# Performance work log

Measured on AMD Instinct MI355X. Metric: run time of the kernel, lower is better.

Reference implementation:

```python
import jax, jax.numpy as jnp
import numpy as np
import math

B, L, OBS, ACT = 2, 1024, 64, 16
OE, AE, RE, TE = 512, 256, 128, 128
C, H, NL, FF = 1024, 16, 4, 4096
DH = C // H


def setup_inputs():
    key = jax.random.key(0)
    ks = jax.random.split(key, 20)
    def nrm(k, shape, std=1.0):
        return jax.random.normal(k, shape, jnp.float32) * std
    kb = jax.random.split(ks[19], 12)
    return {
        'obs_seq': nrm(ks[0], (B, L, OBS)),
        'act_seq': nrm(ks[1], (B, L, ACT)),
        'rew_seq': nrm(ks[2], (B, L, 1)),
        'obs_W': nrm(ks[3], (OBS, OE), OBS ** -0.5), 'obs_b': jnp.zeros((OE,)),
        'act_W': nrm(ks[4], (ACT, AE), ACT ** -0.5), 'act_b': jnp.zeros((AE,)),
        'rew_W': nrm(ks[5], (1, RE), 1.0), 'rew_b': jnp.zeros((RE,)),
        'tr_W': nrm(ks[6], (OBS, TE), OBS ** -0.5), 'tr_b': jnp.zeros((TE,)),
        'bn_gamma': jnp.ones((OBS,)), 'bn_beta': jnp.zeros((OBS,)),
        'ln1_w': jnp.ones((NL, C)), 'ln1_b': jnp.zeros((NL, C)),
        'qkv_W': nrm(kb[0], (NL, C, 3 * C), C ** -0.5), 'qkv_b': jnp.zeros((NL, 3 * C)),
        'out_W': nrm(kb[1], (NL, C, C), C ** -0.5), 'out_b': jnp.zeros((NL, C)),
        'ln2_w': jnp.ones((NL, C)), 'ln2_b': jnp.zeros((NL, C)),
        'fc_W': nrm(kb[2], (NL, C, FF), C ** -0.5), 'fc_b': jnp.zeros((NL, FF)),
        'pj_W': nrm(kb[3], (NL, FF, C), FF ** -0.5), 'pj_b': jnp.zeros((NL, C)),
    }


def _ln(x, w, b):
    m = x.mean(-1, keepdims=True)
    v = ((x - m) ** 2).mean(-1, keepdims=True)
    return (x - m) * jax.lax.rsqrt(v + 1e-5) * w + b


def _forward(obs_seq, act_seq, rew_seq, obs_W, obs_b, act_W, act_b, rew_W, rew_b,
             tr_W, tr_b, bn_gamma, bn_beta, ln1_w, ln1_b, qkv_W, qkv_b, out_W, out_b,
             ln2_w, ln2_b, fc_W, fc_b, pj_W, pj_b):
    # transition branch: prepend first obs, take deltas; BatchNorm1d in training
    # mode uses biased batch stats over (batch, time) per channel.
    full_obs = jnp.concatenate([obs_seq[:, :1], obs_seq], axis=1)  # (B, L+1, OBS)
    obs2 = full_obs[:, :-1]
    tran = full_obs[:, 1:] - full_obs[:, :-1]  # (B, L, OBS)
    tm = tran.mean((0, 1))
    tv = ((tran - tm) ** 2).mean((0, 1))
    tran = (tran - tm) * jax.lax.rsqrt(tv + 1e-5) * bn_gamma + bn_beta
    # encoder_activation is identity
    enc = jnp.concatenate([
        obs2 @ obs_W + obs_b,
        act_seq @ act_W + act_b,
        rew_seq @ rew_W + rew_b,
        tran @ tr_W + tr_b,
    ], axis=-1)  # (B, L, C)
    mask = jnp.tril(jnp.ones((L, L), dtype=bool))

    def block(x, p):
        l1w, l1b, qW, qb, oW, ob, l2w, l2b, fW, fb, pW, pb = p
        h = _ln(x, l1w, l1b)
        q, k, v = jnp.split(h @ qW + qb, 3, axis=-1)
        q, k, v = (t.reshape(B, L, H, DH).transpose(0, 2, 1, 3) for t in (q, k, v))
        s = jnp.einsum('bhqd,bhkd->bhqk', q, k) / math.sqrt(DH)
        s = jnp.where(mask, s, -jnp.inf)
        a = jax.nn.softmax(s, axis=-1)
        o = jnp.einsum('bhqk,bhkd->bhqd', a, v).transpose(0, 2, 1, 3).reshape(B, L, C)
        x = x + o @ oW + ob  # residual + out_proj
        h2 = _ln(x, l2w, l2b)
        x = x + jax.nn.relu(h2 @ fW + fb) @ pW + pb  # MLP residual
        return x, None

    x, _ = jax.lax.scan(block, enc, (ln1_w, ln1_b, qkv_W, qkv_b, out_W, out_b,
                                     ln2_w, ln2_b, fc_W, fc_b, pj_W, pj_b))
    return jnp.tanh(x)


def reference(obs_seq, act_seq, rew_seq, obs_W, obs_b, act_W, act_b, rew_W, rew_b,
              tr_W, tr_b, bn_gamma, bn_beta, ln1_w, ln1_b, qkv_W, qkv_b, out_W, out_b,
              ln2_w, ln2_b, fc_W, fc_b, pj_W, pj_b):
    return _forward(obs_seq, act_seq, rew_seq, obs_W, obs_b, act_W, act_b, rew_W, rew_b,
                    tr_W, tr_b, bn_gamma, bn_beta, ln1_w, ln1_b, qkv_W, qkv_b, out_W, out_b,
                    ln2_w, ln2_b, fc_W, fc_b, pj_W, pj_b)
```

## Files before the change

kernel.cpp:

```cpp
#include <hip/hip_runtime.h>
#include <hip/hip_bf16.h>
#include <math.h>

constexpr int kB   = 2;
constexpr int kL   = 1024;
constexpr int kOBS = 64;
constexpr int kACT = 16;
constexpr int kC   = 1024;
constexpr int kH   = 16;
constexpr int kDH  = 64;
constexpr int kFF  = 4096;
constexpr int kNL  = 4;
constexpr int kRows = kB * kL;
constexpr int kOE = 512, kAE = 256, kRE = 128, kTE = 128;

typedef _Float16 f16x8 __attribute__((ext_vector_type(8)));
typedef _Float16 f16x4 __attribute__((ext_vector_type(4)));
typedef float    f32x4 __attribute__((ext_vector_type(4)));

__device__ __forceinline__ unsigned short f2h(float x) {
    return __builtin_bit_cast(unsigned short, (_Float16)x);
}
__device__ __forceinline__ void gload_lds16(const void* g, void* l) {
    __builtin_amdgcn_global_load_lds(
        (const __attribute__((address_space(1))) unsigned int*)g,
        (__attribute__((address_space(3))) unsigned int*)l, 16, 0, 0);
}

__global__ __launch_bounds__(256) void tran_stats_kernel(
    const float* __restrict__ obs, float* __restrict__ tm, float* __restrict__ tv)
{
    const int f = blockIdx.x;
    const int tid = threadIdx.x;
    float sum = 0.f, sq = 0.f;
    for (int r = tid; r < kRows; r += 256) {
        const int t = r & (kL - 1);
        float d = 0.f;
        if (t > 0) {
            const float cur  = obs[(size_t)r * kOBS + f];
            const float prev = obs[(size_t)(r - 1) * kOBS + f];
            d = cur - prev;
        }
        sum += d; sq += d * d;
    }
    for (int off = 32; off > 0; off >>= 1) {
        sum += __shfl_down(sum, off);
        sq  += __shfl_down(sq, off);
    }
    __shared__ float sa[4], sb[4];
    if ((tid & 63) == 0) { sa[tid >> 6] = sum; sb[tid >> 6] = sq; }
    __syncthreads();
    if (tid == 0) {
        const float ts = sa[0] + sa[1] + sa[2] + sa[3];
        const float tq = sb[0] + sb[1] + sb[2] + sb[3];
        const float m = ts / (float)kRows;
        tm[f] = m;
        tv[f] = tq / (float)kRows - m * m;
    }
}

__global__ __launch_bounds__(256) void encode_kernel(
    const float* __restrict__ obs, const float* __restrict__ act, const float* __restrict__ rew,
    const float* __restrict__ obs_W, const float* __restrict__ obs_b,
    const float* __restrict__ act_W, const float* __restrict__ act_b,
    const float* __restrict__ rew_W, const float* __restrict__ rew_b,
    const float* __restrict__ tr_W,  const float* __restrict__ tr_b,
    const float* __restrict__ bn_g,  const float* __restrict__ bn_b,
    const float* __restrict__ tm,    const float* __restrict__ tv,
    float* __restrict__ enc)
{
    const int row = blockIdx.x;
    const int t = row & (kL - 1);
    const int tid = threadIdx.x;
    __shared__ float s_obs2[kOBS];
    __shared__ float s_tran[kOBS];
    __shared__ float s_act[kACT];
    __shared__ float s_rew;
    if (tid < kOBS) {
        const float cur  = obs[(size_t)row * kOBS + tid];
        const float prev = (t > 0) ? obs[(size_t)(row - 1) * kOBS + tid] : cur;
        s_obs2[tid] = prev;
        const float tr = cur - prev;
        s_tran[tid] = (tr - tm[tid]) * rsqrtf(tv[tid] + 1e-5f) * bn_g[tid] + bn_b[tid];
    } else if (tid < kOBS + kACT) {
        s_act[tid - kOBS] = act[(size_t)row * kACT + (tid - kOBS)];
    } else if (tid == kOBS + kACT) {
        s_rew = rew[row];
    }
    __syncthreads();
    float* er = enc + (size_t)row * kC;
    #pragma unroll
    for (int s = 0; s < 4; ++s) {
        const int c = tid + s * 256;
        float v;
        if (c < kOE) {
            v = obs_b[c];
            #pragma unroll
            for (int k = 0; k < kOBS; ++k) v += s_obs2[k] * obs_W[k * kOE + c];
        } else if (c < kOE + kAE) {
            const int cc = c - kOE;
            v = act_b[cc];
            #pragma unroll
            for (int k = 0; k < kACT; ++k) v += s_act[k] * act_W[k * kAE + cc];
        } else if (c < kOE + kAE + kRE) {
            const int cc = c - (kOE + kAE);
            v = s_rew * rew_W[cc] + rew_b[cc];
        } else {
            const int cc = c - (kOE + kAE + kRE);
            v = tr_b[cc];
            #pragma unroll
            for (int k = 0; k < kOBS; ++k) v += s_tran[k] * tr_W[k * kTE + cc];
        }
        er[c] = v;
    }
}

__global__ __launch_bounds__(256) void ln_kernel(
    const float* __restrict__ x, const float* __restrict__ w,
    const float* __restrict__ b, unsigned short* __restrict__ out)
{
    const int row = blockIdx.x;
    const int tid = threadIdx.x;
    const float4 xv = *reinterpret_cast<const float4*>(&x[(size_t)row * kC + tid * 4]);
    float s = xv.x + xv.y + xv.z + xv.w;
    float q = xv.x * xv.x + xv.y * xv.y + xv.z * xv.z + xv.w * xv.w;
    for (int off = 32; off > 0; off >>= 1) {
        s += __shfl_down(s, off);
        q += __shfl_down(q, off);
    }
    __shared__ float sa[4], sb[4];
    if ((tid & 63) == 0) { sa[tid >> 6] = s; sb[tid >> 6] = q; }
    __syncthreads();
    const float ts = sa[0] + sa[1] + sa[2] + sa[3];
    const float tq = sb[0] + sb[1] + sb[2] + sb[3];
    const float mean = ts * (1.f / kC);
    const float var  = tq * (1.f / kC) - mean * mean;
    const float rstd = rsqrtf(var + 1e-5f);
    const float4 wv = *reinterpret_cast<const float4*>(&w[tid * 4]);
    const float4 bv = *reinterpret_cast<const float4*>(&b[tid * 4]);
    ushort4 o;
    o.x = f2h((xv.x - mean) * rstd * wv.x + bv.x);
    o.y = f2h((xv.y - mean) * rstd * wv.y + bv.y);
    o.z = f2h((xv.z - mean) * rstd * wv.z + bv.z);
    o.w = f2h((xv.w - mean) * rstd * wv.w + bv.w);
    *reinterpret_cast<ushort4*>(&out[(size_t)row * kC + tid * 4]) = o;
}

__device__ __forceinline__ void convT_tile(
    const float* __restrict__ W, unsigned short* __restrict__ WT,
    int K, int N, int k0, int n0, int tid)
{
    __shared__ unsigned short t[64][68];
    const int r = tid >> 4, c4 = (tid & 15) * 4;
    #pragma unroll
    for (int s = 0; s < 4; ++s) {
        const int rr = r + s * 16;
        const float4 v = *reinterpret_cast<const float4*>(&W[(size_t)(k0 + rr) * N + n0 + c4]);
        t[rr][c4 + 0] = f2h(v.x);
        t[rr][c4 + 1] = f2h(v.y);
        t[rr][c4 + 2] = f2h(v.z);
        t[rr][c4 + 3] = f2h(v.w);
    }
    __syncthreads();
    #pragma unroll
    for (int s = 0; s < 4; ++s) {
        const int rn = r + s * 16;
        ushort4 o;
        o.x = t[c4 + 0][rn];
        o.y = t[c4 + 1][rn];
        o.z = t[c4 + 2][rn];
        o.w = t[c4 + 3][rn];
        *reinterpret_cast<ushort4*>(&WT[(size_t)(n0 + rn) * K + k0 + c4]) = o;
    }
}

__global__ __launch_bounds__(256) void convert_layer_kernel(
    const float* __restrict__ qW, const float* __restrict__ oW,
    const float* __restrict__ fW, const float* __restrict__ pW,
    unsigned short* __restrict__ qWT, unsigned short* __restrict__ oWT,
    unsigned short* __restrict__ fWT, unsigned short* __restrict__ pWT)
{
    int bid = blockIdx.x;
    const int tid = threadIdx.x;
    if (bid < 768)  {
        convT_tile(qW, qWT, 1024, 3072, (bid / 48) * 64, (bid % 48) * 64, tid);
    } else if (bid < 1024) {
        bid -= 768;
        convT_tile(oW, oWT, 1024, 1024, (bid / 16) * 64, (bid % 16) * 64, tid);
    } else if (bid < 2048) {
        bid -= 1024;
        convT_tile(fW, fWT, 1024, 4096, (bid / 64) * 64, (bid % 64) * 64, tid);
    } else {
        bid -= 2048;
        convT_tile(pW, pWT, 4096, 1024, (bid / 16) * 64, (bid % 16) * 64, tid);
    }
}

template<int RELU, int RES, int MODE>
__global__ __launch_bounds__(256) void gemm_f16_kernel(
    const unsigned short* __restrict__ A,
    const unsigned short* __restrict__ BT,
    const float* __restrict__ bias,
    float* __restrict__ Cf, unsigned short* __restrict__ Ch,
    unsigned short* __restrict__ Cv,
    int M, int N, int K)
{
    __shared__ __align__(16) unsigned short As[2][128 * 64];
    __shared__ __align__(16) unsigned short Bs[2][128 * 64];
    const int tid = threadIdx.x;
    const int lane = tid & 63;
    const int wv   = tid >> 6;
    const int wr = wv >> 1, wc = wv & 1;

    const int nx  = gridDim.x;
    const int nxy = gridDim.x * gridDim.y;
    int flat = blockIdx.x + nx * blockIdx.y + nxy * blockIdx.z;
    const int cpx = (nxy * gridDim.z) >> 3;
    flat = (flat & 7) * cpx + (flat >> 3);
    const int bx = flat % nx;
    const int by = (flat / nx) % gridDim.y;
    const int bz = flat / nxy;

    const int bm = by * 128;
    const int bn = bx * 128;
    const int ksz  = K / gridDim.z;
    const int kbeg = bz * ksz;
    const int kend = kbeg + ksz;

    const int grow = tid >> 3;
    const int gs   = (tid & 7) ^ (grow & 7);

    const int fr = lane & 15;
    const int kb = lane >> 4;

    auto stage = [&](int k0, int buf) {
        #pragma unroll
        for (int c = 0; c < 4; ++c) {
            gload_lds16(A  + (size_t)(bm + c * 32 + grow) * K + k0 + gs * 8,
                        (char*)&As[buf][0] + c * 4096 + wv * 1024);
            gload_lds16(BT + (size_t)(bn + c * 32 + grow) * K + k0 + gs * 8,
                        (char*)&Bs[buf][0] + c * 4096 + wv * 1024);
        }
    };

    f32x4 acc[4][4] = {};

    stage(kbeg, 0);
    __syncthreads();
    int cur = 0;
    for (int k0 = kbeg; k0 < kend; k0 += 64) {
        f16x8 a[2][4], b[2][4];
        #pragma unroll
        for (int kf = 0; kf < 2; ++kf) {
            #pragma unroll
            for (int m = 0; m < 4; ++m) {
                const int row = wr * 64 + m * 16 + fr;
                a[kf][m] = *reinterpret_cast<const f16x8*>(
                    &As[cur][row * 64 + (((kf * 4 + kb) ^ (row & 7)) * 8)]);
            }
            #pragma unroll
            for (int n = 0; n < 4; ++n) {
                const int row = wc * 64 + n * 16 + fr;
                b[kf][n] = *reinterpret_cast<const f16x8*>(
                    &Bs[cur][row * 64 + (((kf * 4 + kb) ^ (row & 7)) * 8)]);
            }
        }
        if (k0 + 64 < kend) stage(k0 + 64, cur ^ 1);
        #pragma unroll
        for (int kf = 0; kf < 2; ++kf)
            #pragma unroll
            for (int m = 0; m < 4; ++m)
                #pragma unroll
                for (int n = 0; n < 4; ++n)
                    acc[m][n] = __builtin_amdgcn_mfma_f32_16x16x32_f16(
                        a[kf][m], b[kf][n], acc[m][n], 0, 0, 0);

        __syncthreads();
        cur ^= 1;
    }

    const int fq = lane >> 4;
    if (MODE == 4) {
        const bool addb = (bz == 0);
        #pragma unroll
        for (int n = 0; n < 4; ++n) {
            const int c = bn + wc * 64 + n * 16 + fr;
            const float bv = addb ? bias[c] : 0.f;
            #pragma unroll
            for (int m = 0; m < 4; ++m) {
                #pragma unroll
                for (int j = 0; j < 4; ++j) {
                    const int r = bm + wr * 64 + m * 16 + fq * 4 + j;
                    atomicAdd(&Cf[(size_t)r * N + c], acc[m][n][j] + bv);
                }
            }
        }
        return;
    }
    if (MODE == 2) {
        if (bn < 2 * kC) {
            #pragma unroll
            for (int n = 0; n < 4; ++n) {
                const int c = bn + wc * 64 + n * 16 + fr;
                const float bv = bias[c];
                #pragma unroll
                for (int m = 0; m < 4; ++m) {
                    #pragma unroll
                    for (int j = 0; j < 4; ++j) {
                        const int r = bm + wr * 64 + m * 16 + fq * 4 + j;
                        Ch[(size_t)r * (2 * kC) + c] = f2h(acc[m][n][j] + bv);
                    }
                }
            }
        } else {
            #pragma unroll
            for (int n = 0; n < 4; ++n) {
                const int c  = bn + wc * 64 + n * 16 + fr;
                const int cc = c - 2 * kC;
                const int hh = cc >> 6, dd = cc & 63;
                const float bv = bias[c];
                #pragma unroll
                for (int m = 0; m < 4; ++m) {
                    const int rr = bm + wr * 64 + m * 16 + fq * 4;
                    const int bb = rr >> 10, t0 = rr & 1023;
                    f16x4 pk;
                    #pragma unroll
                    for (int j = 0; j < 4; ++j) pk[j] = (_Float16)(acc[m][n][j] + bv);
                    *reinterpret_cast<f16x4*>(
                        &Cv[((size_t)(bb * kH + hh) * kDH + dd) * kL + t0]) = pk;
                }
            }
        }
        return;
    }
    #pragma unroll
    for (int n = 0; n < 4; ++n) {
        const int c = bn + wc * 64 + n * 16 + fr;
        const float bv = bias[c];
        #pragma unroll
        for (int m = 0; m < 4; ++m) {
            #pragma unroll
            for (int j = 0; j < 4; ++j) {
                const int r = bm + wr * 64 + m * 16 + fq * 4 + j;
                float v = acc[m][n][j] + bv;
                if (RES)  v += Cf[(size_t)r * N + c];
                if (RELU) v = fmaxf(v, 0.f);
                if (MODE == 1) Ch[(size_t)r * N + c] = f2h(v);
                else           Cf[(size_t)r * N + c] = v;
            }
        }
    }
}

__device__ __forceinline__ int swz(int row, int slot) {
    return row * 64 + ((slot ^ (row & 7)) * 8);
}

__global__ __launch_bounds__(256) void attn_mfma_kernel(
    const unsigned short* __restrict__ qk,
    const unsigned short* __restrict__ vt,
    unsigned short* __restrict__ o)
{
    const int bid = blockIdx.x;
    const int bh  = bid & 31;
    const int qb  = ((bid >> 5) + bh) & 15;
    const int b   = bh >> 4;
    const int h   = bh & 15;
    const int tid  = threadIdx.x;
    const int lane = tid & 63;
    const int wv   = tid >> 6;
    const int fr = lane & 15;
    const int g  = lane >> 4;

    __shared__ __align__(16) unsigned short Ks[64 * 64];
    __shared__ __align__(16) unsigned short Vts[64 * 64];
    __shared__ __align__(16) unsigned short Ps[64 * 64];

    const int qlo = qb * 64;
    const int qg_row = qlo + wv * 16 + fr;

    f16x8 qfrag[2];
    {
        const unsigned short* qg = &qk[(size_t)(b * kL + qg_row) * (2 * kC) + h * kDH];
        #pragma unroll
        for (int kf = 0; kf < 2; ++kf) {
            f16x8 v = *reinterpret_cast<const f16x8*>(&qg[(kf * 4 + g) * 8]);
            #pragma unroll
            for (int i = 0; i < 8; ++i) v[i] *= (_Float16)0.125f;
            qfrag[kf] = v;
        }
    }

    const int sr = tid >> 2;
    const int ss = tid & 3;
    const unsigned short* kbase = &qk[(size_t)(b * kL) * (2 * kC) + kC + h * kDH];
    const unsigned short* vbase = &vt[(size_t)(b * kH + h) * kDH * kL];

    f16x8 kc0 = *reinterpret_cast<const f16x8*>(&kbase[(size_t)sr * (2 * kC) + ss * 8]);
    f16x8 kc1 = *reinterpret_cast<const f16x8*>(&kbase[(size_t)sr * (2 * kC) + (ss + 4) * 8]);
    f16x8 vc0 = *reinterpret_cast<const f16x8*>(&vbase[(size_t)sr * kL + ss * 8]);
    f16x8 vc1 = *reinterpret_cast<const f16x8*>(&vbase[(size_t)sr * kL + (ss + 4) * 8]);

    float m = -INFINITY, l = 0.f;
    f32x4 acc_o[4] = {};

    for (int k0 = 0; k0 <= qlo; k0 += 64) {
        asm volatile("s_waitcnt lgkmcnt(0)" ::: "memory");
        __builtin_amdgcn_sched_barrier(0);
        __builtin_amdgcn_s_barrier();
        __builtin_amdgcn_sched_barrier(0);

        *reinterpret_cast<f16x8*>(&Ks[swz(sr, ss)])      = kc0;
        *reinterpret_cast<f16x8*>(&Ks[swz(sr, ss + 4)])  = kc1;
        *reinterpret_cast<f16x8*>(&Vts[swz(sr, ss)])     = vc0;
        *reinterpret_cast<f16x8*>(&Vts[swz(sr, ss + 4)]) = vc1;

        if (k0 + 64 <= qlo) {
            kc0 = *reinterpret_cast<const f16x8*>(&kbase[(size_t)(k0 + 64 + sr) * (2 * kC) + ss * 8]);
            kc1 = *reinterpret_cast<const f16x8*>(&kbase[(size_t)(k0 + 64 + sr) * (2 * kC) + (ss + 4) * 8]);
            vc0 = *reinterpret_cast<const f16x8*>(&vbase[(size_t)sr * kL + k0 + 64 + ss * 8]);
            vc1 = *reinterpret_cast<const f16x8*>(&vbase[(size_t)sr * kL + k0 + 64 + (ss + 4) * 8]);
        }

        asm volatile("s_waitcnt lgkmcnt(0)" ::: "memory");
        __builtin_amdgcn_sched_barrier(0);
        __builtin_amdgcn_s_barrier();
        __builtin_amdgcn_sched_barrier(0);

        f32x4 acc_s[4] = {};
        #pragma unroll
        for (int kf = 0; kf < 2; ++kf) {
            #pragma unroll
            for (int n = 0; n < 4; ++n) {
                const f16x8 kfr = *reinterpret_cast<const f16x8*>(&Ks[swz(n * 16 + fr, kf * 4 + g)]);
                acc_s[n] = __builtin_amdgcn_mfma_f32_16x16x32_f16(kfr, qfrag[kf], acc_s[n], 0, 0, 0);
            }
        }

        if (k0 == qlo) {
            #pragma unroll
            for (int n = 0; n < 4; ++n)
                #pragma unroll
                for (int j = 0; j < 4; ++j)
                    if (k0 + n * 16 + g * 4 + j > qg_row) acc_s[n][j] = -INFINITY;
        }

        float mx = -INFINITY;
        #pragma unroll
        for (int n = 0; n < 4; ++n)
            #pragma unroll
            for (int j = 0; j < 4; ++j) mx = fmaxf(mx, acc_s[n][j]);
        mx = fmaxf(mx, __shfl_xor(mx, 16));
        mx = fmaxf(mx, __shfl_xor(mx, 32));
        const float mn  = fmaxf(m, mx);
        const float fac = __expf(m - mn);
        float p[4][4];
        float psum = 0.f;
        #pragma unroll
        for (int n = 0; n < 4; ++n)
            #pragma unroll
            for (int j = 0; j < 4; ++j) { p[n][j] = __expf(acc_s[n][j] - mn); psum += p[n][j]; }
        psum += __shfl_xor(psum, 16);
        psum += __shfl_xor(psum, 32);
        l = l * fac + psum;
        m = mn;
        #pragma unroll
        for (int dt = 0; dt < 4; ++dt)
            #pragma unroll
            for (int j = 0; j < 4; ++j) acc_o[dt][j] *= fac;

        #pragma unroll
        for (int n = 0; n < 4; ++n) {
            f16x4 pk;
            #pragma unroll
            for (int j = 0; j < 4; ++j) pk[j] = (_Float16)p[n][j];
            *reinterpret_cast<f16x4*>(&Ps[swz(wv * 16 + fr, 2 * n + (g >> 1)) + (g & 1) * 4]) = pk;
        }

        #pragma unroll
        for (int kf = 0; kf < 2; ++kf) {
            const f16x8 pf = *reinterpret_cast<const f16x8*>(&Ps[swz(wv * 16 + fr, kf * 4 + g)]);
            #pragma unroll
            for (int dt = 0; dt < 4; ++dt) {
                const f16x8 vf = *reinterpret_cast<const f16x8*>(&Vts[swz(dt * 16 + fr, kf * 4 + g)]);
                acc_o[dt] = __builtin_amdgcn_mfma_f32_16x16x32_f16(vf, pf, acc_o[dt], 0, 0, 0);
            }
        }
    }

    const float rl = 1.f / l;
    unsigned short* ob = &o[(size_t)(b * kL + qg_row) * kC + h * kDH];
    #pragma unroll
    for (int dt = 0; dt < 4; ++dt) {
        f16x4 pk;
        #pragma unroll
        for (int j = 0; j < 4; ++j) pk[j] = (_Float16)(acc_o[dt][j] * rl);
        *reinterpret_cast<f16x4*>(&ob[dt * 16 + g * 4]) = pk;
    }
}

__global__ __launch_bounds__(256) void tanh_kernel(float* __restrict__ x)
{
    const size_t i = ((size_t)blockIdx.x * 256 + threadIdx.x) * 4;
    float4 v = *reinterpret_cast<float4*>(&x[i]);
    v.x = tanhf(v.x); v.y = tanhf(v.y); v.z = tanhf(v.z); v.w = tanhf(v.w);
    *reinterpret_cast<float4*>(&x[i]) = v;
}

extern "C" void kernel_launch(void* const* d_in, const int* in_sizes, int n_in,
                              void* d_out, int out_size, void* d_ws, size_t ws_size,
                              hipStream_t stream)
{
    (void)in_sizes; (void)n_in; (void)out_size; (void)ws_size;
    const float* obs    = (const float*)d_in[0];
    const float* act    = (const float*)d_in[1];
    const float* rew    = (const float*)d_in[2];
    const float* obs_W  = (const float*)d_in[3];
    const float* obs_b  = (const float*)d_in[4];
    const float* act_W  = (const float*)d_in[5];
    const float* act_b  = (const float*)d_in[6];
    const float* rew_W  = (const float*)d_in[7];
    const float* rew_b  = (const float*)d_in[8];
    const float* tr_W   = (const float*)d_in[9];
    const float* tr_b   = (const float*)d_in[10];
    const float* bn_g   = (const float*)d_in[11];
    const float* bn_b   = (const float*)d_in[12];
    const float* ln1_w  = (const float*)d_in[13];
    const float* ln1_b  = (const float*)d_in[14];
    const float* qkv_W  = (const float*)d_in[15];
    const float* qkv_b  = (const float*)d_in[16];
    const float* out_W  = (const float*)d_in[17];
    const float* out_b  = (const float*)d_in[18];
    const float* ln2_w  = (const float*)d_in[19];
    const float* ln2_b  = (const float*)d_in[20];
    const float* fc_W   = (const float*)d_in[21];
    const float* fc_b   = (const float*)d_in[22];
    const float* pj_W   = (const float*)d_in[23];
    const float* pj_b   = (const float*)d_in[24];

    float* x  = (float*)d_out;
    float* ws = (float*)d_ws;
    float* tm   = ws;
    float* tv   = ws + 64;
    unsigned short* wbuf  = (unsigned short*)(ws + 128);
    unsigned short* h_hf  = wbuf + 12582912;
    unsigned short* ao_hf = h_hf + (size_t)kRows * kC;
    unsigned short* ff_hf = ao_hf + (size_t)kRows * kC;
    unsigned short* qk_hf = ff_hf + (size_t)kRows * kFF;
    unsigned short* vt_hf = qk_hf + (size_t)kRows * 2 * kC;
    unsigned short* qWT = wbuf;
    unsigned short* oWT = qWT + 3 * kC * kC;
    unsigned short* fWT = oWT + kC * kC;
    unsigned short* pWT = fWT + kC * kFF;

    tran_stats_kernel<<<kOBS, 256, 0, stream>>>(obs, tm, tv);
    encode_kernel<<<kRows, 256, 0, stream>>>(obs, act, rew,
        obs_W, obs_b, act_W, act_b, rew_W, rew_b, tr_W, tr_b, bn_g, bn_b, tm, tv, x);

    for (int lyr = 0; lyr < kNL; ++lyr) {
        const float* qW = qkv_W + (size_t)lyr * kC * 3 * kC;
        const float* qB = qkv_b + (size_t)lyr * 3 * kC;
        const float* oW = out_W + (size_t)lyr * kC * kC;
        const float* oB = out_b + (size_t)lyr * kC;
        const float* fW = fc_W + (size_t)lyr * kC * kFF;
        const float* fB = fc_b + (size_t)lyr * kFF;
        const float* pW = pj_W + (size_t)lyr * kFF * kC;
        const float* pB = pj_b + (size_t)lyr * kC;

        convert_layer_kernel<<<3072, 256, 0, stream>>>(
            qW, oW, fW, pW, qWT, oWT, fWT, pWT);

        ln_kernel<<<kRows, 256, 0, stream>>>(x, ln1_w + lyr * kC, ln1_b + lyr * kC, h_hf);
        gemm_f16_kernel<0,0,2><<<dim3(3 * kC / 128, kRows / 128), 256, 0, stream>>>(
            h_hf, qWT, qB, nullptr, qk_hf, vt_hf, kRows, 3 * kC, kC);
        attn_mfma_kernel<<<dim3(512), 256, 0, stream>>>(qk_hf, vt_hf, ao_hf);
        gemm_f16_kernel<0,0,4><<<dim3(kC / 128, kRows / 128, 4), 256, 0, stream>>>(
            ao_hf, oWT, oB, x, nullptr, nullptr, kRows, kC, kC);
        ln_kernel<<<kRows, 256, 0, stream>>>(x, ln2_w + lyr * kC, ln2_b + lyr * kC, h_hf);
        gemm_f16_kernel<1,0,1><<<dim3(kFF / 128, kRows / 128), 256, 0, stream>>>(
            h_hf, fWT, fB, nullptr, ff_hf, nullptr, kRows, kFF, kC);
        gemm_f16_kernel<0,0,4><<<dim3(kC / 128, kRows / 128, 4), 256, 0, stream>>>(
            ff_hf, pWT, pB, x, nullptr, nullptr, kRows, kC, kFF);
    }
    tanh_kernel<<<kRows * kC / 1024, 256, 0, stream>>>(x);
}
```

Baseline: 671.6 us.

## Replace split-K atomics with fp16 partial buffers reduced inside fused LayerNorm

The split-K out-projection and MLP down-projection GEMMs no longer atomically add fp32 results into the residual. Each K-slice now writes its fp16 partial to a separate buffer that reuses the qk workspace. A new kernel sums the four partials into the residual and applies the next LayerNorm in the same pass, and a variant fuses the final sum with tanh. This removes atomic traffic and a separate LN/tanh pass, but the partials are rounded to fp16 before summation, which costs some accuracy.

```diff
diff --git a/kernel.cpp b/kernel.cpp
--- a/kernel.cpp
+++ b/kernel.cpp
@@ -20,6 +20,9 @@
 
 __device__ __forceinline__ unsigned short f2h(float x) {
     return __builtin_bit_cast(unsigned short, (_Float16)x);
+}
+__device__ __forceinline__ float h2f(unsigned short x) {
+    return (float)__builtin_bit_cast(_Float16, x);
 }
 __device__ __forceinline__ void gload_lds16(const void* g, void* l) {
     __builtin_amdgcn_global_load_lds(
@@ -146,6 +149,62 @@
     *reinterpret_cast<ushort4*>(&out[(size_t)row * kC + tid * 4]) = o;
 }
 
+__global__ __launch_bounds__(256) void reduce_ln_kernel(
+    const unsigned short* __restrict__ part,
+    const float* __restrict__ w, const float* __restrict__ b,
+    float* __restrict__ x, unsigned short* __restrict__ h)
+{
+    const int row = blockIdx.x;
+    const int tid = threadIdx.x;
+    const size_t base = (size_t)row * kC + tid * 4;
+    float4 xv = *reinterpret_cast<const float4*>(&x[base]);
+    #pragma unroll
+    for (int z = 0; z < 4; ++z) {
+        const ushort4 p = *reinterpret_cast<const ushort4*>(
+            &part[(size_t)z * kRows * kC + base]);
+        xv.x += h2f(p.x); xv.y += h2f(p.y); xv.z += h2f(p.z); xv.w += h2f(p.w);
+    }
+    *reinterpret_cast<float4*>(&x[base]) = xv;
+
+    float s = xv.x + xv.y + xv.z + xv.w;
+    float q = xv.x * xv.x + xv.y * xv.y + xv.z * xv.z + xv.w * xv.w;
+    for (int off = 32; off > 0; off >>= 1) {
+        s += __shfl_down(s, off);
+        q += __shfl_down(q, off);
+    }
+    __shared__ float sa[4], sb[4];
+    if ((tid & 63) == 0) { sa[tid >> 6] = s; sb[tid >> 6] = q; }
+    __syncthreads();
+    const float ts = sa[0] + sa[1] + sa[2] + sa[3];
+    const float tq = sb[0] + sb[1] + sb[2] + sb[3];
+    const float mean = ts * (1.f / kC);
+    const float var  = tq * (1.f / kC) - mean * mean;
+    const float rstd = rsqrtf(var + 1e-5f);
+    const float4 wv = *reinterpret_cast<const float4*>(&w[tid * 4]);
+    const float4 bv = *reinterpret_cast<const float4*>(&b[tid * 4]);
+    ushort4 o;
+    o.x = f2h((xv.x - mean) * rstd * wv.x + bv.x);
+    o.y = f2h((xv.y - mean) * rstd * wv.y + bv.y);
+    o.z = f2h((xv.z - mean) * rstd * wv.z + bv.z);
+    o.w = f2h((xv.w - mean) * rstd * wv.w + bv.w);
+    *reinterpret_cast<ushort4*>(&h[base]) = o;
+}
+
+__global__ __launch_bounds__(256) void reduce_tanh_kernel(
+    const unsigned short* __restrict__ part, float* __restrict__ x)
+{
+    const size_t base = ((size_t)blockIdx.x * 256 + threadIdx.x) * 4;
+    float4 xv = *reinterpret_cast<const float4*>(&x[base]);
+    #pragma unroll
+    for (int z = 0; z < 4; ++z) {
+        const ushort4 p = *reinterpret_cast<const ushort4*>(
+            &part[(size_t)z * kRows * kC + base]);
+        xv.x += h2f(p.x); xv.y += h2f(p.y); xv.z += h2f(p.z); xv.w += h2f(p.w);
+    }
+    xv.x = tanhf(xv.x); xv.y = tanhf(xv.y); xv.z = tanhf(xv.z); xv.w = tanhf(xv.w);
+    *reinterpret_cast<float4*>(&x[base]) = xv;
+}
+
 __device__ __forceinline__ void convT_tile(
     const float* __restrict__ W, unsigned short* __restrict__ WT,
     int K, int N, int k0, int n0, int tid)
@@ -280,7 +339,8 @@
     }
 
     const int fq = lane >> 4;
-    if (MODE == 4) {
+    if (MODE == 5) {
+        unsigned short* pp = Ch + (size_t)bz * M * N;
         const bool addb = (bz == 0);
         #pragma unroll
         for (int n = 0; n < 4; ++n) {
@@ -291,7 +351,7 @@
                 #pragma unroll
                 for (int j = 0; j < 4; ++j) {
                     const int r = bm + wr * 64 + m * 16 + fq * 4 + j;
-                    atomicAdd(&Cf[(size_t)r * N + c], acc[m][n][j] + bv);
+                    pp[(size_t)r * N + c] = f2h(acc[m][n][j] + bv);
                 }
             }
         }
@@ -497,14 +557,6 @@
         for (int j = 0; j < 4; ++j) pk[j] = (_Float16)(acc_o[dt][j] * rl);
         *reinterpret_cast<f16x4*>(&ob[dt * 16 + g * 4]) = pk;
     }
-}
-
-__global__ __launch_bounds__(256) void tanh_kernel(float* __restrict__ x)
-{
-    const size_t i = ((size_t)blockIdx.x * 256 + threadIdx.x) * 4;
-    float4 v = *reinterpret_cast<float4*>(&x[i]);
-    v.x = tanhf(v.x); v.y = tanhf(v.y); v.z = tanhf(v.z); v.w = tanhf(v.w);
-    *reinterpret_cast<float4*>(&x[i]) = v;
 }
 
 extern "C" void kernel_launch(void* const* d_in, const int* in_sizes, int n_in,
@@ -548,6 +600,7 @@
     unsigned short* ff_hf = ao_hf + (size_t)kRows * kC;
     unsigned short* qk_hf = ff_hf + (size_t)kRows * kFF;
     unsigned short* vt_hf = qk_hf + (size_t)kRows * 2 * kC;
+    unsigned short* part  = qk_hf;
     unsigned short* qWT = wbuf;
     unsigned short* oWT = qWT + 3 * kC * kC;
     unsigned short* fWT = oWT + kC * kC;
@@ -556,6 +609,7 @@
     tran_stats_kernel<<<kOBS, 256, 0, stream>>>(obs, tm, tv);
     encode_kernel<<<kRows, 256, 0, stream>>>(obs, act, rew,
         obs_W, obs_b, act_W, act_b, rew_W, rew_b, tr_W, tr_b, bn_g, bn_b, tm, tv, x);
+    ln_kernel<<<kRows, 256, 0, stream>>>(x, ln1_w, ln1_b, h_hf);
 
     for (int lyr = 0; lyr < kNL; ++lyr) {
         const float* qW = qkv_W + (size_t)lyr * kC * 3 * kC;
@@ -570,17 +624,22 @@
         convert_layer_kernel<<<3072, 256, 0, stream>>>(
             qW, oW, fW, pW, qWT, oWT, fWT, pWT);
 
-        ln_kernel<<<kRows, 256, 0, stream>>>(x, ln1_w + lyr * kC, ln1_b + lyr * kC, h_hf);
         gemm_f16_kernel<0,0,2><<<dim3(3 * kC / 128, kRows / 128), 256, 0, stream>>>(
             h_hf, qWT, qB, nullptr, qk_hf, vt_hf, kRows, 3 * kC, kC);
         attn_mfma_kernel<<<dim3(512), 256, 0, stream>>>(qk_hf, vt_hf, ao_hf);
-        gemm_f16_kernel<0,0,4><<<dim3(kC / 128, kRows / 128, 4), 256, 0, stream>>>(
-            ao_hf, oWT, oB, x, nullptr, nullptr, kRows, kC, kC);
-        ln_kernel<<<kRows, 256, 0, stream>>>(x, ln2_w + lyr * kC, ln2_b + lyr * kC, h_hf);
+        gemm_f16_kernel<0,0,5><<<dim3(kC / 128, kRows / 128, 4), 256, 0, stream>>>(
+            ao_hf, oWT, oB, nullptr, part, nullptr, kRows, kC, kC);
+        reduce_ln_kernel<<<kRows, 256, 0, stream>>>(
+            part, ln2_w + lyr * kC, ln2_b + lyr * kC, x, h_hf);
         gemm_f16_kernel<1,0,1><<<dim3(kFF / 128, kRows / 128), 256, 0, stream>>>(
             h_hf, fWT, fB, nullptr, ff_hf, nullptr, kRows, kFF, kC);
-        gemm_f16_kernel<0,0,4><<<dim3(kC / 128, kRows / 128, 4), 256, 0, stream>>>(
-            ff_hf, pWT, pB, x, nullptr, nullptr, kRows, kC, kFF);
-    }
-    tanh_kernel<<<kRows * kC / 1024, 256, 0, stream>>>(x);
-}
+        gemm_f16_kernel<0,0,5><<<dim3(kC / 128, kRows / 128, 4), 256, 0, stream>>>(
+            ff_hf, pWT, pB, nullptr, part, nullptr, kRows, kC, kFF);
+        if (lyr < kNL - 1) {
+            reduce_ln_kernel<<<kRows, 256, 0, stream>>>(
+                part, ln1_w + (lyr + 1) * kC, ln1_b + (lyr + 1) * kC, x, h_hf);
+        } else {
+            reduce_tanh_kernel<<<kRows * kC / 1024, 256, 0, stream>>>(part, x);
+        }
+    }
+}
```

Measured after the change: 553.8 us. 1.21x faster.
